# Kernel tuning notes

Hardware: AMD Instinct MI355X
Metric: run time of the kernel (lower is better)

## Reference

```python
import jax, jax.numpy as jnp
import numpy as np

EPS = 1e-5  # BatchNorm eps

def conv1x1(x, w, b):
    # x: [B,C,H,W], w: [O,C], b: [O]
    return jnp.einsum('bchw,oc->bohw', x, w) + b[None, :, None, None]

def bn(x, s, b, m, v):
    # eval-mode BatchNorm2d with running stats m,v
    inv = s * jax.lax.rsqrt(v + EPS)
    return x * inv[None, :, None, None] + (b - m * inv)[None, :, None, None]

def maxpool2(x):
    B, C, H, W = x.shape
    return x.reshape(B, C, H // 2, 2, W // 2, 2).max(axis=(3, 5))

def setup_inputs() -> dict:
    key = jax.random.key(0)
    ks = jax.random.split(key, 32)
    B, CH, H, W = 8, 64, 64, 64
    cq, cv = CH // 8, CH // 2
    r = lambda k, sh: jax.random.normal(k, sh, dtype=jnp.float32)
    u = lambda k, sh: jax.random.uniform(k, sh, dtype=jnp.float32)
    return {
        'x': r(ks[0], (B, CH, H, W)),
        'memory': r(ks[1], (B, CH, H, W)),
        'wq': r(ks[2], (cq, CH)) * 0.1, 'bq': r(ks[3], (cq,)) * 0.1,
        'bnq_s': u(ks[4], (cq,)), 'bnq_b': r(ks[5], (cq,)) * 0.1,
        'bnq_m': r(ks[6], (cq,)) * 0.1, 'bnq_v': u(ks[7], (cq,)),
        'wk': r(ks[8], (cq, CH)) * 0.1, 'bk': r(ks[9], (cq,)) * 0.1,
        'bnk_s': u(ks[10], (cq,)), 'bnk_b': r(ks[11], (cq,)) * 0.1,
        'bnk_m': r(ks[12], (cq,)) * 0.1, 'bnk_v': u(ks[13], (cq,)),
        'wv': r(ks[14], (cv, CH)) * 0.1, 'bv': r(ks[15], (cv,)) * 0.1,
        'bnv_s': u(ks[16], (cv,)), 'bnv_b': r(ks[17], (cv,)) * 0.1,
        'bnv_m': r(ks[18], (cv,)) * 0.1, 'bnv_v': u(ks[19], (cv,)),
        'wp': r(ks[20], (CH, cv)) * 0.1, 'bp': r(ks[21], (CH,)) * 0.1,
        'bnp_s': u(ks[22], (CH,)), 'bnp_b': r(ks[23], (CH,)) * 0.1,
        'bnp_m': r(ks[24], (CH,)) * 0.1, 'bnp_v': u(ks[25], (CH,)),
        'gamma': r(ks[26], (1,)),
    }

def reference(x, memory, wq, bq, bnq_s, bnq_b, bnq_m, bnq_v,
              wk, bk, bnk_s, bnk_b, bnk_m, bnk_v,
              wv, bv, bnv_s, bnv_b, bnv_m, bnv_v,
              wp, bp, bnp_s, bnp_b, bnp_m, bnp_v, gamma):
    B, CH, H, W = x.shape
    cq, cv = CH // 8, CH // 2
    HW, HW4 = H * W, (H * W) // 4
    # query from full-res memory: [B, HW, cq]
    q = bn(conv1x1(memory, wq, bq), bnq_s, bnq_b, bnq_m, bnq_v)
    q = q.reshape(B, cq, HW).transpose(0, 2, 1)
    # key pooled: [B, cq, HW/4]
    k = maxpool2(bn(conv1x1(memory, wk, bk), bnk_s, bnk_b, bnk_m, bnk_v))
    k = k.reshape(B, cq, HW4)
    # attention: [B, HW, HW/4], softmax over last dim (no scaling, as in source)
    attn = jax.nn.softmax(jnp.einsum('bnc,bcm->bnm', q, k), axis=2)
    # value pooled: [B, HW/4, cv]
    v = maxpool2(bn(conv1x1(memory, wv, bv), bnv_s, bnv_b, bnv_m, bnv_v))
    v = v.reshape(B, cv, HW4).transpose(0, 2, 1)
    # attn_g: [B, HW, cv] -> [B, cv, H, W]
    g = jnp.einsum('bnm,bmc->bnc', attn, v).transpose(0, 2, 1).reshape(B, cv, H, W)
    g = bn(conv1x1(g, wp, bp), bnp_s, bnp_b, bnp_m, bnp_v)
    return x + gamma * g
```

## Files before the change

kernel.cpp:

```cpp
#include <hip/hip_runtime.h>

#define EPS_BN 1e-5f

constexpr int Bn   = 8;
constexpr int CHn  = 64;
constexpr int HWn  = 4096;
constexpr int HW4n = 1024;
constexpr int CQn  = 8;
constexpr int CVn  = 32;

typedef short bf16x8 __attribute__((ext_vector_type(8)));
typedef float f32x4  __attribute__((ext_vector_type(4)));

union FragI { int4 i; bf16x8 v; };

__device__ __forceinline__ unsigned short f2bf(float f) {
    unsigned u = __float_as_uint(f);
    unsigned r = u + 0x7FFFu + ((u >> 16) & 1u);
    return (unsigned short)(r >> 16);
}
__device__ __forceinline__ float bf2f(unsigned short h) {
    return __uint_as_float(((unsigned)h) << 16);
}

__device__ __align__(16) short g_Kh[Bn * HW4n * CQn];
__device__ __align__(16) short g_Kl[Bn * HW4n * CQn];
__device__ __align__(16) short g_Vt[Bn * CVn * HW4n];

__global__ __launch_bounds__(192)
void k_proj_kv(const float* __restrict__ mem,
               const float* __restrict__ wk,  const float* __restrict__ bk,
               const float* __restrict__ ks,  const float* __restrict__ kb,
               const float* __restrict__ km,  const float* __restrict__ kv,
               const float* __restrict__ wv,  const float* __restrict__ bv_,
               const float* __restrict__ vs,  const float* __restrict__ vb,
               const float* __restrict__ vm,  const float* __restrict__ vv)
{
    __shared__ float wall[2560];
    __shared__ float beta[40];
    __shared__ float Msh[8192];

    const int tid = threadIdx.x;
    for (int idx = tid; idx < 2560; idx += 192) {
        int c = idx % 40, ch = idx / 40;
        float w, inv;
        if (c < 8) { inv = ks[c] * rsqrtf(kv[c] + EPS_BN); w = wk[c * 64 + ch]; }
        else { int c2 = c - 8; inv = vs[c2] * rsqrtf(vv[c2] + EPS_BN); w = wv[c2 * 64 + ch]; }
        wall[ch * 40 + c] = w * inv;
    }
    if (tid < 40) {
        int c = tid;
        if (c < 8) {
            float inv = ks[c] * rsqrtf(kv[c] + EPS_BN);
            beta[c] = (bk[c] - km[c]) * inv + kb[c];
        } else {
            int c2 = c - 8;
            float inv = vs[c2] * rsqrtf(vv[c2] + EPS_BN);
            beta[c] = (bv_[c2] - vm[c2]) * inv + vb[c2];
        }
    }

    const int b = blockIdx.x >> 5;
    const int R = blockIdx.x & 31;

    {
        const float* src = mem + (size_t)b * (CHn * HWn) + (R << 7);
        for (int idx = tid; idx < 4096; idx += 192) {
            int ch = idx >> 6, p2 = idx & 63;
            float2 v = *(const float2*)(src + ch * HWn + (p2 << 1));
            int r = p2 >> 5, w2 = p2 & 31;
            *(float2*)&Msh[ch * 128 + (w2 << 2) + (r << 1)] = v;
        }
    }
    __syncthreads();

    if (tid < 160) {
        const int g  = tid % 5;
        const int qd = tid / 5;
        float acc[4][8];
        #pragma unroll
        for (int p = 0; p < 4; ++p)
            #pragma unroll
            for (int c = 0; c < 8; ++c) acc[p][c] = 0.f;

        for (int ch = 0; ch < 64; ++ch) {
            const float4 mq = *(const float4*)&Msh[ch * 128 + (qd << 2)];
            const float4* wr = (const float4*)&wall[ch * 40 + (g << 3)];
            const float4 w0 = wr[0], w1 = wr[1];
            #pragma unroll
            for (int p = 0; p < 4; ++p) {
                const float mv = (p == 0) ? mq.x : (p == 1) ? mq.y : (p == 2) ? mq.z : mq.w;
                acc[p][0] = fmaf(w0.x, mv, acc[p][0]); acc[p][1] = fmaf(w0.y, mv, acc[p][1]);
                acc[p][2] = fmaf(w0.z, mv, acc[p][2]); acc[p][3] = fmaf(w0.w, mv, acc[p][3]);
                acc[p][4] = fmaf(w1.x, mv, acc[p][4]); acc[p][5] = fmaf(w1.y, mv, acc[p][5]);
                acc[p][6] = fmaf(w1.z, mv, acc[p][6]); acc[p][7] = fmaf(w1.w, mv, acc[p][7]);
            }
        }
        float o[8];
        #pragma unroll
        for (int c = 0; c < 8; ++c)
            o[c] = fmaxf(fmaxf(acc[0][c], acc[1][c]), fmaxf(acc[2][c], acc[3][c]))
                 + beta[(g << 3) + c];

        const int m = (R << 5) + qd;
        if (g == 0) {
            unsigned short hb[8], lb[8];
            #pragma unroll
            for (int c = 0; c < 8; ++c) {
                hb[c] = f2bf(o[c]);
                lb[c] = f2bf(o[c] - bf2f(hb[c]));
            }
            int4 hi4 = make_int4((int)(hb[0] | ((unsigned)hb[1] << 16)),
                                 (int)(hb[2] | ((unsigned)hb[3] << 16)),
                                 (int)(hb[4] | ((unsigned)hb[5] << 16)),
                                 (int)(hb[6] | ((unsigned)hb[7] << 16)));
            int4 lo4 = make_int4((int)(lb[0] | ((unsigned)lb[1] << 16)),
                                 (int)(lb[2] | ((unsigned)lb[3] << 16)),
                                 (int)(lb[4] | ((unsigned)lb[5] << 16)),
                                 (int)(lb[6] | ((unsigned)lb[7] << 16)));
            *(int4*)&g_Kh[((size_t)b * HW4n + m) * CQn] = hi4;
            *(int4*)&g_Kl[((size_t)b * HW4n + m) * CQn] = lo4;
        } else {
            const int ch0 = (g - 1) << 3;
            #pragma unroll
            for (int c = 0; c < 8; ++c)
                g_Vt[(size_t)b * (CVn * HW4n) + (ch0 + c) * HW4n + m] = (short)f2bf(o[c]);
        }
    }
}

__global__ __launch_bounds__(256, 2) __attribute__((amdgpu_waves_per_eu(2, 2)))
void k_attn7(const float* __restrict__ mem,
             const float* __restrict__ x,
             const float* __restrict__ wq, const float* __restrict__ bq,
             const float* __restrict__ qs, const float* __restrict__ qb,
             const float* __restrict__ qm, const float* __restrict__ qv,
             const float* __restrict__ wp, const float* __restrict__ bp,
             const float* __restrict__ ps, const float* __restrict__ pb,
             const float* __restrict__ pm, const float* __restrict__ pv,
             const float* __restrict__ gamma,
             float* __restrict__ out)
{
    __shared__ __align__(16) short Kh_sh[HW4n * CQn];
    __shared__ __align__(16) short Kl_sh[HW4n * CQn];
    __shared__ __align__(16) short Vt_sh[2][32 * 136];
    __shared__ __align__(16) short Psh[2][4 * 16 * 40];
    __shared__ __align__(16) float qw_sh[512];
    __shared__ float qbeta_sh[8];
    __shared__ float pbeta_sh[64];

    const int tid  = threadIdx.x;
    const int lane = tid & 63;
    const int w    = tid >> 6;
    const int quad = lane >> 4;
    const int c    = lane & 15;
    const int b    = blockIdx.x >> 6;
    const int tile = blockIdx.x & 63;
    const float gm = gamma[0];

    for (int idx = tid; idx < 512; idx += 256) {
        int cc = idx & 7, ch = idx >> 3;
        float inv = qs[cc] * rsqrtf(qv[cc] + EPS_BN);
        qw_sh[ch * 8 + cc] = wq[cc * 64 + ch] * inv;
    }
    if (tid < 8) {
        float inv = qs[tid] * rsqrtf(qv[tid] + EPS_BN);
        qbeta_sh[tid] = (bq[tid] - qm[tid]) * inv + qb[tid];
    }
    if (tid < 64) {
        float inv = ps[tid] * rsqrtf(pv[tid] + EPS_BN);
        pbeta_sh[tid] = gm * ((bp[tid] - pm[tid]) * inv + pb[tid]);
    }
    const short* Vsrc = g_Vt + (size_t)b * (CVn * HW4n);
    {
        const int4* Kh4 = (const int4*)(g_Kh + (size_t)b * (HW4n * CQn));
        const int4* Kl4 = (const int4*)(g_Kl + (size_t)b * (HW4n * CQn));
        int4* dh = (int4*)Kh_sh;
        int4* dl = (int4*)Kl_sh;
        #pragma unroll
        for (int i = 0; i < 4; ++i) {
            dh[tid + i * 256] = Kh4[tid + i * 256];
            dl[tid + i * 256] = Kl4[tid + i * 256];
        }
        #pragma unroll
        for (int i = 0; i < 2; ++i) {
            int idx4 = tid + (i << 8);
            int ch = idx4 >> 4, k8 = idx4 & 15;
            *(int4*)&Vt_sh[0][ch * 136 + (k8 << 3)] = *(const int4*)(Vsrc + ch * HW4n + (k8 << 3));
        }
    }
    __syncthreads();

    float q0 = 0.f, q1 = 0.f, q2 = 0.f, q3 = 0.f, q4 = 0.f, q5 = 0.f, q6 = 0.f, q7 = 0.f;
    {
        const float* mp = mem + (size_t)b * (CHn * HWn) + (tile << 6) + (w << 4) + c;
        #pragma unroll
        for (int cc = 0; cc < 16; ++cc) {
            const int ch = (quad << 4) | cc;
            const float mv = mp[ch * HWn];
            const float4 w0 = *(const float4*)&qw_sh[ch * 8];
            const float4 w1 = *(const float4*)&qw_sh[ch * 8 + 4];
            q0 = fmaf(w0.x, mv, q0); q1 = fmaf(w0.y, mv, q1);
            q2 = fmaf(w0.z, mv, q2); q3 = fmaf(w0.w, mv, q3);
            q4 = fmaf(w1.x, mv, q4); q5 = fmaf(w1.y, mv, q5);
            q6 = fmaf(w1.z, mv, q6); q7 = fmaf(w1.w, mv, q7);
        }
        q0 += __shfl_xor(q0, 16); q0 += __shfl_xor(q0, 32); q0 += qbeta_sh[0];
        q1 += __shfl_xor(q1, 16); q1 += __shfl_xor(q1, 32); q1 += qbeta_sh[1];
        q2 += __shfl_xor(q2, 16); q2 += __shfl_xor(q2, 32); q2 += qbeta_sh[2];
        q3 += __shfl_xor(q3, 16); q3 += __shfl_xor(q3, 32); q3 += qbeta_sh[3];
        q4 += __shfl_xor(q4, 16); q4 += __shfl_xor(q4, 32); q4 += qbeta_sh[4];
        q5 += __shfl_xor(q5, 16); q5 += __shfl_xor(q5, 32); q5 += qbeta_sh[5];
        q6 += __shfl_xor(q6, 16); q6 += __shfl_xor(q6, 32); q6 += qbeta_sh[6];
        q7 += __shfl_xor(q7, 16); q7 += __shfl_xor(q7, 32); q7 += qbeta_sh[7];
    }
    bf16x8 bqsel;
    {
        unsigned short h0 = f2bf(q0), h1 = f2bf(q1), h2 = f2bf(q2), h3 = f2bf(q3);
        unsigned short h4 = f2bf(q4), h5 = f2bf(q5), h6 = f2bf(q6), h7 = f2bf(q7);
        unsigned short l0 = f2bf(q0 - bf2f(h0)), l1 = f2bf(q1 - bf2f(h1));
        unsigned short l2 = f2bf(q2 - bf2f(h2)), l3 = f2bf(q3 - bf2f(h3));
        unsigned short l4 = f2bf(q4 - bf2f(h4)), l5 = f2bf(q5 - bf2f(h5));
        unsigned short l6 = f2bf(q6 - bf2f(h6)), l7 = f2bf(q7 - bf2f(h7));
        FragI fh, fl;
        fh.i = make_int4((int)(h0 | ((unsigned)h1 << 16)), (int)(h2 | ((unsigned)h3 << 16)),
                         (int)(h4 | ((unsigned)h5 << 16)), (int)(h6 | ((unsigned)h7 << 16)));
        fl.i = make_int4((int)(l0 | ((unsigned)l1 << 16)), (int)(l2 | ((unsigned)l3 << 16)),
                         (int)(l4 | ((unsigned)l5 << 16)), (int)(l6 | ((unsigned)l7 << 16)));
        bqsel = (quad & 1) ? fl.v : fh.v;
    }
    const short* Krow = (quad < 2) ? Kh_sh : Kl_sh;

    f32x4 acc0 = {0.f, 0.f, 0.f, 0.f};
    f32x4 acc1 = {0.f, 0.f, 0.f, 0.f};
    float m_ = -3.0e38f, l_ = 0.f;

    const int pbase = w * 640 + c * 40;
    const int pread = w * 640 + c * 40 + (quad << 3);

    for (int chunk = 0; chunk < 8; ++chunk) {
        const int cur = chunk & 1;
        if (chunk < 7) {
            const short* Vn = Vsrc + ((chunk + 1) << 7);
            #pragma unroll
            for (int i = 0; i < 2; ++i) {
                int idx4 = tid + (i << 8);
                int ch = idx4 >> 4, k8 = idx4 & 15;
                *(int4*)&Vt_sh[cur ^ 1][ch * 136 + (k8 << 3)] = *(const int4*)(Vn + ch * HW4n + (k8 << 3));
            }
        }
        #pragma unroll
        for (int st = 0; st < 4; ++st) {
            const int kb   = (chunk << 7) + (st << 5);
            const int kloc = st << 5;
            const int pbuf = st & 1;

            f32x4 sa = {0.f, 0.f, 0.f, 0.f};
            f32x4 sb = {0.f, 0.f, 0.f, 0.f};
            {
                const bf16x8 a0 = *(const bf16x8*)&Krow[(kb + c) * 8];
                sa = __builtin_amdgcn_mfma_f32_16x16x32_bf16(a0, bqsel, sa, 0, 0, 0);
                const bf16x8 a1 = *(const bf16x8*)&Krow[(kb + 16 + c) * 8];
                sb = __builtin_amdgcn_mfma_f32_16x16x32_bf16(a1, bqsel, sb, 0, 0, 0);
            }

            float mx = fmaxf(fmaxf(fmaxf(sa[0], sa[1]), fmaxf(sa[2], sa[3])),
                             fmaxf(fmaxf(sb[0], sb[1]), fmaxf(sb[2], sb[3])));
            mx = fmaxf(mx, m_);
            mx = fmaxf(mx, __shfl_xor(mx, 16));
            mx = fmaxf(mx, __shfl_xor(mx, 32));
            const float alpha = __expf(m_ - mx);
            m_ = mx;
            const float pa0 = __expf(sa[0] - mx), pa1 = __expf(sa[1] - mx);
            const float pa2 = __expf(sa[2] - mx), pa3 = __expf(sa[3] - mx);
            const float pb0 = __expf(sb[0] - mx), pb1 = __expf(sb[1] - mx);
            const float pb2 = __expf(sb[2] - mx), pb3 = __expf(sb[3] - mx);
            l_ = l_ * alpha + (pa0 + pa1 + pa2 + pa3 + pb0 + pb1 + pb2 + pb3);

            *(int*)&Psh[pbuf][pbase + (quad << 2)]          = (int)(f2bf(pa0) | ((unsigned)f2bf(pa1) << 16));
            *(int*)&Psh[pbuf][pbase + (quad << 2) + 2]      = (int)(f2bf(pa2) | ((unsigned)f2bf(pa3) << 16));
            *(int*)&Psh[pbuf][pbase + 16 + (quad << 2)]     = (int)(f2bf(pb0) | ((unsigned)f2bf(pb1) << 16));
            *(int*)&Psh[pbuf][pbase + 16 + (quad << 2) + 2] = (int)(f2bf(pb2) | ((unsigned)f2bf(pb3) << 16));

            const float a0 = __shfl(alpha, 20 * quad + 0);
            const float a1 = __shfl(alpha, 20 * quad + 1);
            const float a2 = __shfl(alpha, 20 * quad + 2);
            const float a3 = __shfl(alpha, 20 * quad + 3);
            acc0[0] *= a0; acc0[1] *= a1; acc0[2] *= a2; acc0[3] *= a3;
            acc1[0] *= a0; acc1[1] *= a1; acc1[2] *= a2; acc1[3] *= a3;

            const bf16x8 pfrag = *(const bf16x8*)&Psh[pbuf][pread];
            const bf16x8 v0 = *(const bf16x8*)&Vt_sh[cur][c * 136 + kloc + (quad << 3)];
            const bf16x8 v1 = *(const bf16x8*)&Vt_sh[cur][(16 + c) * 136 + kloc + (quad << 3)];
            acc0 = __builtin_amdgcn_mfma_f32_16x16x32_bf16(pfrag, v0, acc0, 0, 0, 0);
            acc1 = __builtin_amdgcn_mfma_f32_16x16x32_bf16(pfrag, v1, acc1, 0, 0, 0);
        }
        __syncthreads();
    }

    float* wpf = (float*)Vt_sh;
    for (int idx = tid; idx < 2048; idx += 256) {
        int o = idx >> 5, cc = idx & 31;
        float inv = ps[o] * rsqrtf(pv[o] + EPS_BN);
        wpf[o * 36 + cc] = wp[o * 32 + cc] * inv * gm;
    }

    {
        l_ += __shfl_xor(l_, 16);
        l_ += __shfl_xor(l_, 32);
        const float rl = 1.0f / l_;
        const float r0 = __shfl(rl, 20 * quad + 0);
        const float r1 = __shfl(rl, 20 * quad + 1);
        const float r2 = __shfl(rl, 20 * quad + 2);
        const float r3 = __shfl(rl, 20 * quad + 3);
        float* Gsh = (float*)Kh_sh;
        const int row = (w << 4) + (quad << 2);
        Gsh[(row + 0) * 36 + c] = acc0[0] * r0;
        Gsh[(row + 1) * 36 + c] = acc0[1] * r1;
        Gsh[(row + 2) * 36 + c] = acc0[2] * r2;
        Gsh[(row + 3) * 36 + c] = acc0[3] * r3;
        Gsh[(row + 0) * 36 + 16 + c] = acc1[0] * r0;
        Gsh[(row + 1) * 36 + 16 + c] = acc1[1] * r1;
        Gsh[(row + 2) * 36 + 16 + c] = acc1[2] * r2;
        Gsh[(row + 3) * 36 + 16 + c] = acc1[3] * r3;
    }
    __syncthreads();

    {
        const float* Gsh = (const float*)Kh_sh;
        const int q = tid >> 2, r = tid & 3;
        const float4* gq4 = (const float4*)&Gsh[q * 36];
        float g[32];
        #pragma unroll
        for (int i = 0; i < 8; ++i) {
            const float4 gv = gq4[i];
            g[4*i+0] = gv.x; g[4*i+1] = gv.y; g[4*i+2] = gv.z; g[4*i+3] = gv.w;
        }
        const int n = (tile << 6) + q;
        const float* xp = x + (size_t)b * (CHn * HWn) + n;
        float* op = out + (size_t)b * (CHn * HWn) + n;

        #pragma unroll
        for (int oo = 0; oo < 16; ++oo) {
            const int o = (oo << 2) | r;
            const float4* wr = (const float4*)&wpf[o * 36];
            float po = pbeta_sh[o];
            #pragma unroll
            for (int c4 = 0; c4 < 8; ++c4) {
                const float4 ww = wr[c4];
                po += ww.x * g[4*c4] + ww.y * g[4*c4+1] + ww.z * g[4*c4+2] + ww.w * g[4*c4+3];
            }
            op[o * HWn] = xp[o * HWn] + po;
        }
    }
}

extern "C" void kernel_launch(void* const* d_in, const int* in_sizes, int n_in,
                              void* d_out, int out_size, void* d_ws, size_t ws_size,
                              hipStream_t stream)
{
    const float* x    = (const float*)d_in[0];
    const float* mem  = (const float*)d_in[1];
    const float* wq   = (const float*)d_in[2];
    const float* bq   = (const float*)d_in[3];
    const float* bnqs = (const float*)d_in[4];
    const float* bnqb = (const float*)d_in[5];
    const float* bnqm = (const float*)d_in[6];
    const float* bnqv = (const float*)d_in[7];
    const float* wk   = (const float*)d_in[8];
    const float* bk   = (const float*)d_in[9];
    const float* bnks = (const float*)d_in[10];
    const float* bnkb = (const float*)d_in[11];
    const float* bnkm = (const float*)d_in[12];
    const float* bnkv = (const float*)d_in[13];
    const float* wv   = (const float*)d_in[14];
    const float* bv   = (const float*)d_in[15];
    const float* bnvs = (const float*)d_in[16];
    const float* bnvb = (const float*)d_in[17];
    const float* bnvm = (const float*)d_in[18];
    const float* bnvv = (const float*)d_in[19];
    const float* wp   = (const float*)d_in[20];
    const float* bp   = (const float*)d_in[21];
    const float* bnps = (const float*)d_in[22];
    const float* bnpb = (const float*)d_in[23];
    const float* bnpm = (const float*)d_in[24];
    const float* bnpv = (const float*)d_in[25];
    const float* gam  = (const float*)d_in[26];

    (void)d_ws; (void)ws_size; (void)in_sizes; (void)n_in; (void)out_size;

    k_proj_kv<<<dim3(256), dim3(192), 0, stream>>>(mem,
        wk, bk, bnks, bnkb, bnkm, bnkv,
        wv, bv, bnvs, bnvb, bnvm, bnvv);
    k_attn7<<<dim3(512), dim3(256), 0, stream>>>(mem, x,
        wq, bq, bnqs, bnqb, bnqm, bnqv,
        wp, bp, bnps, bnpb, bnpm, bnpv, gam,
        (float*)d_out);
}
```

Measured before the change: 154.4 us.

## Use two-pass softmax with precomputed row max and direct global V loads

Replaces the online softmax with two passes: a first QK^T sweep computes the exact row maximum, then a second sweep recomputes scores, exponentiates against the fixed max and accumulates PV. This removes the per-step alpha rescaling, cross-lane max shuffles and per-chunk block barriers. V fragments are now read directly from global memory (L2) instead of being staged through double-buffered shared memory, which frees LDS and drops the in-loop syncthreads. In exchange the QK MFMAs run twice, and V loads are uncoalesced per-lane global reads whose latency is no longer hidden by explicit staging.

```diff
diff --git a/kernel.cpp b/kernel.cpp
--- a/kernel.cpp
+++ b/kernel.cpp
@@ -130,7 +130,7 @@
 }
 
 __global__ __launch_bounds__(256, 2) __attribute__((amdgpu_waves_per_eu(2, 2)))
-void k_attn7(const float* __restrict__ mem,
+void k_attn8(const float* __restrict__ mem,
              const float* __restrict__ x,
              const float* __restrict__ wq, const float* __restrict__ bq,
              const float* __restrict__ qs, const float* __restrict__ qb,
@@ -143,7 +143,6 @@
 {
     __shared__ __align__(16) short Kh_sh[HW4n * CQn];
     __shared__ __align__(16) short Kl_sh[HW4n * CQn];
-    __shared__ __align__(16) short Vt_sh[2][32 * 136];
     __shared__ __align__(16) short Psh[2][4 * 16 * 40];
     __shared__ __align__(16) float qw_sh[512];
     __shared__ float qbeta_sh[8];
@@ -171,7 +170,6 @@
         float inv = ps[tid] * rsqrtf(pv[tid] + EPS_BN);
         pbeta_sh[tid] = gm * ((bp[tid] - pm[tid]) * inv + pb[tid]);
     }
-    const short* Vsrc = g_Vt + (size_t)b * (CVn * HW4n);
     {
         const int4* Kh4 = (const int4*)(g_Kh + (size_t)b * (HW4n * CQn));
         const int4* Kl4 = (const int4*)(g_Kl + (size_t)b * (HW4n * CQn));
@@ -181,12 +179,6 @@
         for (int i = 0; i < 4; ++i) {
             dh[tid + i * 256] = Kh4[tid + i * 256];
             dl[tid + i * 256] = Kl4[tid + i * 256];
-        }
-        #pragma unroll
-        for (int i = 0; i < 2; ++i) {
-            int idx4 = tid + (i << 8);
-            int ch = idx4 >> 4, k8 = idx4 & 15;
-            *(int4*)&Vt_sh[0][ch * 136 + (k8 << 3)] = *(const int4*)(Vsrc + ch * HW4n + (k8 << 3));
         }
     }
     __syncthreads();
@@ -231,74 +223,61 @@
     }
     const short* Krow = (quad < 2) ? Kh_sh : Kl_sh;
 
+    float Mloc = -3.0e38f;
+    #pragma unroll 4
+    for (int st = 0; st < 32; ++st) {
+        const int kb = st << 5;
+        f32x4 sa = {0.f, 0.f, 0.f, 0.f};
+        f32x4 sb = {0.f, 0.f, 0.f, 0.f};
+        const bf16x8 a0 = *(const bf16x8*)&Krow[(kb + c) * 8];
+        sa = __builtin_amdgcn_mfma_f32_16x16x32_bf16(a0, bqsel, sa, 0, 0, 0);
+        const bf16x8 a1 = *(const bf16x8*)&Krow[(kb + 16 + c) * 8];
+        sb = __builtin_amdgcn_mfma_f32_16x16x32_bf16(a1, bqsel, sb, 0, 0, 0);
+        const float ma = fmaxf(fmaxf(sa[0], sa[1]), fmaxf(sa[2], sa[3]));
+        const float mb = fmaxf(fmaxf(sb[0], sb[1]), fmaxf(sb[2], sb[3]));
+        Mloc = fmaxf(Mloc, fmaxf(ma, mb));
+    }
+    Mloc = fmaxf(Mloc, __shfl_xor(Mloc, 16));
+    Mloc = fmaxf(Mloc, __shfl_xor(Mloc, 32));
+    const float M = Mloc;
+
+    float l_ = 0.f;
     f32x4 acc0 = {0.f, 0.f, 0.f, 0.f};
     f32x4 acc1 = {0.f, 0.f, 0.f, 0.f};
-    float m_ = -3.0e38f, l_ = 0.f;
-
+    const short* Vrow0 = g_Vt + (size_t)b * (CVn * HW4n) + c * HW4n + (quad << 3);
+    const short* Vrow1 = Vrow0 + 16 * HW4n;
     const int pbase = w * 640 + c * 40;
     const int pread = w * 640 + c * 40 + (quad << 3);
 
-    for (int chunk = 0; chunk < 8; ++chunk) {
-        const int cur = chunk & 1;
-        if (chunk < 7) {
-            const short* Vn = Vsrc + ((chunk + 1) << 7);
-            #pragma unroll
-            for (int i = 0; i < 2; ++i) {
-                int idx4 = tid + (i << 8);
-                int ch = idx4 >> 4, k8 = idx4 & 15;
-                *(int4*)&Vt_sh[cur ^ 1][ch * 136 + (k8 << 3)] = *(const int4*)(Vn + ch * HW4n + (k8 << 3));
-            }
-        }
-        #pragma unroll
-        for (int st = 0; st < 4; ++st) {
-            const int kb   = (chunk << 7) + (st << 5);
-            const int kloc = st << 5;
-            const int pbuf = st & 1;
-
-            f32x4 sa = {0.f, 0.f, 0.f, 0.f};
-            f32x4 sb = {0.f, 0.f, 0.f, 0.f};
-            {
-                const bf16x8 a0 = *(const bf16x8*)&Krow[(kb + c) * 8];
-                sa = __builtin_amdgcn_mfma_f32_16x16x32_bf16(a0, bqsel, sa, 0, 0, 0);
-                const bf16x8 a1 = *(const bf16x8*)&Krow[(kb + 16 + c) * 8];
-                sb = __builtin_amdgcn_mfma_f32_16x16x32_bf16(a1, bqsel, sb, 0, 0, 0);
-            }
-
-            float mx = fmaxf(fmaxf(fmaxf(sa[0], sa[1]), fmaxf(sa[2], sa[3])),
-                             fmaxf(fmaxf(sb[0], sb[1]), fmaxf(sb[2], sb[3])));
-            mx = fmaxf(mx, m_);
-            mx = fmaxf(mx, __shfl_xor(mx, 16));
-            mx = fmaxf(mx, __shfl_xor(mx, 32));
-            const float alpha = __expf(m_ - mx);
-            m_ = mx;
-            const float pa0 = __expf(sa[0] - mx), pa1 = __expf(sa[1] - mx);
-            const float pa2 = __expf(sa[2] - mx), pa3 = __expf(sa[3] - mx);
-            const float pb0 = __expf(sb[0] - mx), pb1 = __expf(sb[1] - mx);
-            const float pb2 = __expf(sb[2] - mx), pb3 = __expf(sb[3] - mx);
-            l_ = l_ * alpha + (pa0 + pa1 + pa2 + pa3 + pb0 + pb1 + pb2 + pb3);
-
-            *(int*)&Psh[pbuf][pbase + (quad << 2)]          = (int)(f2bf(pa0) | ((unsigned)f2bf(pa1) << 16));
-            *(int*)&Psh[pbuf][pbase + (quad << 2) + 2]      = (int)(f2bf(pa2) | ((unsigned)f2bf(pa3) << 16));
-            *(int*)&Psh[pbuf][pbase + 16 + (quad << 2)]     = (int)(f2bf(pb0) | ((unsigned)f2bf(pb1) << 16));
-            *(int*)&Psh[pbuf][pbase + 16 + (quad << 2) + 2] = (int)(f2bf(pb2) | ((unsigned)f2bf(pb3) << 16));
-
-            const float a0 = __shfl(alpha, 20 * quad + 0);
-            const float a1 = __shfl(alpha, 20 * quad + 1);
-            const float a2 = __shfl(alpha, 20 * quad + 2);
-            const float a3 = __shfl(alpha, 20 * quad + 3);
-            acc0[0] *= a0; acc0[1] *= a1; acc0[2] *= a2; acc0[3] *= a3;
-            acc1[0] *= a0; acc1[1] *= a1; acc1[2] *= a2; acc1[3] *= a3;
-
-            const bf16x8 pfrag = *(const bf16x8*)&Psh[pbuf][pread];
-            const bf16x8 v0 = *(const bf16x8*)&Vt_sh[cur][c * 136 + kloc + (quad << 3)];
-            const bf16x8 v1 = *(const bf16x8*)&Vt_sh[cur][(16 + c) * 136 + kloc + (quad << 3)];
-            acc0 = __builtin_amdgcn_mfma_f32_16x16x32_bf16(pfrag, v0, acc0, 0, 0, 0);
-            acc1 = __builtin_amdgcn_mfma_f32_16x16x32_bf16(pfrag, v1, acc1, 0, 0, 0);
-        }
-        __syncthreads();
-    }
-
-    float* wpf = (float*)Vt_sh;
+    #pragma unroll 2
+    for (int st = 0; st < 32; ++st) {
+        const int kb = st << 5;
+        const bf16x8 v0 = *(const bf16x8*)(Vrow0 + kb);
+        const bf16x8 v1 = *(const bf16x8*)(Vrow1 + kb);
+        f32x4 sa = {0.f, 0.f, 0.f, 0.f};
+        f32x4 sb = {0.f, 0.f, 0.f, 0.f};
+        const bf16x8 a0 = *(const bf16x8*)&Krow[(kb + c) * 8];
+        sa = __builtin_amdgcn_mfma_f32_16x16x32_bf16(a0, bqsel, sa, 0, 0, 0);
+        const bf16x8 a1 = *(const bf16x8*)&Krow[(kb + 16 + c) * 8];
+        sb = __builtin_amdgcn_mfma_f32_16x16x32_bf16(a1, bqsel, sb, 0, 0, 0);
+        const float pa0 = __expf(sa[0] - M), pa1 = __expf(sa[1] - M);
+        const float pa2 = __expf(sa[2] - M), pa3 = __expf(sa[3] - M);
+        const float pb0 = __expf(sb[0] - M), pb1 = __expf(sb[1] - M);
+        const float pb2 = __expf(sb[2] - M), pb3 = __expf(sb[3] - M);
+        l_ += ((pa0 + pa1) + (pa2 + pa3)) + ((pb0 + pb1) + (pb2 + pb3));
+        const int pbuf = st & 1;
+        *(int*)&Psh[pbuf][pbase + (quad << 2)]          = (int)(f2bf(pa0) | ((unsigned)f2bf(pa1) << 16));
+        *(int*)&Psh[pbuf][pbase + (quad << 2) + 2]      = (int)(f2bf(pa2) | ((unsigned)f2bf(pa3) << 16));
+        *(int*)&Psh[pbuf][pbase + 16 + (quad << 2)]     = (int)(f2bf(pb0) | ((unsigned)f2bf(pb1) << 16));
+        *(int*)&Psh[pbuf][pbase + 16 + (quad << 2) + 2] = (int)(f2bf(pb2) | ((unsigned)f2bf(pb3) << 16));
+        const bf16x8 pfrag = *(const bf16x8*)&Psh[pbuf][pread];
+        acc0 = __builtin_amdgcn_mfma_f32_16x16x32_bf16(pfrag, v0, acc0, 0, 0, 0);
+        acc1 = __builtin_amdgcn_mfma_f32_16x16x32_bf16(pfrag, v1, acc1, 0, 0, 0);
+    }
+
+    __syncthreads();
+
+    float* wpf = (float*)Kl_sh;
     for (int idx = tid; idx < 2048; idx += 256) {
         int o = idx >> 5, cc = idx & 31;
         float inv = ps[o] * rsqrtf(pv[o] + EPS_BN);
@@ -392,7 +371,7 @@
     k_proj_kv<<<dim3(256), dim3(192), 0, stream>>>(mem,
         wk, bk, bnks, bnkb, bnkm, bnkv,
         wv, bv, bnvs, bnvb, bnvm, bnvv);
-    k_attn7<<<dim3(512), dim3(256), 0, stream>>>(mem, x,
+    k_attn8<<<dim3(512), dim3(256), 0, stream>>>(mem, x,
         wq, bq, bnqs, bnqb, bnqm, bnqv,
         wp, bp, bnps, bnpb, bnpm, bnpv, gam,
         (float*)d_out);
```

Result: no change. 152.5 us (-1.3%).
